# Optimization experiments

Measured on AMD Instinct MI355X. Metric: run time of the kernel, lower is better.

The kernel has to match this reference:

```python
import jax, jax.numpy as jnp
import numpy as np

N_NODE = 100000
EMB = 112
NNZ = 1000000
B = 512
L = 50
LAYERS = 2


def setup_inputs() -> dict:
    key = jax.random.key(0)
    ks = jax.random.split(key, 9)
    embedding = jax.random.normal(ks[0], (N_NODE, EMB), dtype=jnp.float32) * 0.1
    adj_vals = jax.random.uniform(ks[1], (NNZ,), dtype=jnp.float32)
    adj_rows = jax.random.randint(ks[2], (NNZ,), 0, N_NODE, dtype=jnp.int32)
    adj_cols = jax.random.randint(ks[3], (NNZ,), 0, N_NODE, dtype=jnp.int32)
    D = jax.random.normal(ks[4], (B, B), dtype=jnp.float32) * (1.0 / B)
    A = jax.random.normal(ks[5], (B, B), dtype=jnp.float32)
    session_item = jax.random.randint(ks[6], (B, L), 0, N_NODE + 1, dtype=jnp.int32)  # 0 = pad row
    session_len = jnp.floor(jax.random.uniform(ks[7], (B, 1), dtype=jnp.float32) * (L - 1)) + 1.0
    stdv = 1.0 / np.sqrt(EMB)
    w_sess = jax.random.normal(ks[8], (LAYERS, EMB, EMB), dtype=jnp.float32) * stdv
    return {"embedding": embedding, "adj_vals": adj_vals, "adj_rows": adj_rows,
            "adj_cols": adj_cols, "D": D, "A": A, "session_item": session_item,
            "session_len": session_len, "w_sess": w_sess}


def _l2_normalize(x, eps=1e-12):
    n = jnp.linalg.norm(x, axis=-1, keepdims=True)
    return x / jnp.maximum(n, eps)


def _hyperconv(embedding, adj_vals, adj_rows, adj_cols):
    # mean over layer outputs of repeated sparse.mm(adjacency, embedding)
    cur = embedding
    acc = embedding
    for _ in range(LAYERS):
        msgs = adj_vals[:, None] * cur[adj_cols]           # [nnz, E] gather
        cur = jax.ops.segment_sum(msgs, adj_rows, num_segments=N_NODE)
        acc = acc + cur
    return acc / (LAYERS + 1)


def _sessconv(item_emb, D, A, session_item, session_len, w_sess):
    pad_emb = jnp.concatenate([jnp.zeros((1, EMB), item_emb.dtype), item_emb], axis=0)
    seq_h = pad_emb[session_item]                           # [B, L, E] gather (vectorized index_select loop)
    sess = jnp.sum(seq_h, axis=1) / session_len             # [B, E] mean pool
    DA = D @ A                                              # [B, B]
    acc = sess
    for i in range(LAYERS):
        sess = sess @ w_sess[i].T                           # Linear, no bias
        sess = DA @ sess
        sess = _l2_normalize(sess)
        acc = acc + sess
    return acc / (LAYERS + 1)


def reference(embedding, adj_vals, adj_rows, adj_cols, D, A, session_item, session_len, w_sess):
    item_emb = _hyperconv(embedding, adj_vals, adj_rows, adj_cols)
    sess_emb = _sessconv(item_emb, D, A, session_item, session_len, w_sess)
    return sess_emb
```

## Files before the change

### kernel.cpp

```cpp
#include <hip/hip_runtime.h>
#include <hip/hip_bf16.h>

#define N_NODE 100000
#define EMB 112
#define EMBQ 28
#define EMBQ4 14
#define NNZ 1000000
#define BATCH 512
#define SEQL 50

typedef unsigned int uint32;

__device__ __forceinline__ unsigned short f2bf(float f) {
    uint32 u = __float_as_uint(f);
    u = (u + 0x7fffu + ((u >> 16) & 1u)) >> 16;
    return (unsigned short)u;
}
__device__ __forceinline__ uint32 pack_bf2(float x, float y) {
    return (uint32)f2bf(x) | ((uint32)f2bf(y) << 16);
}
__device__ __forceinline__ float2 unpack_bf2(uint32 p) {
    float2 r;
    r.x = __uint_as_float(p << 16);
    r.y = __uint_as_float(p & 0xffff0000u);
    return r;
}

#define NPAD 100352
#define NBUCKET 196
#define BCAP 6144
#define CHUNK 2048
#define MS_BLOCKS 489
#define MAXC 25600
#define POISON ((int)0xAAAAAAAA)

__global__ __launch_bounds__(256)
void split_prep_kernel(const int* __restrict__ rows,
                       const int* __restrict__ cols,
                       const float* __restrict__ vals,
                       int* __restrict__ cur, int2* __restrict__ tmp,
                       const float4* __restrict__ embf4,
                       uint2* __restrict__ embb2,
                       const int* __restrict__ items,
                       int* __restrict__ flags, int* __restrict__ mapv,
                       int* __restrict__ rlist, int* __restrict__ cntp) {
    __shared__ int hist[NBUCKET];
    __shared__ int lexcl[NBUCKET];
    __shared__ int gbase[NBUCKET];
    __shared__ int lcur[NBUCKET];
    __shared__ int sscan[256];
    __shared__ unsigned char sbuck[CHUNK];
    __shared__ int2 stage[CHUNK];
    int t = threadIdx.x;
    if (blockIdx.x < MS_BLOCKS) {
        int base = blockIdx.x * CHUNK;
        int m = NNZ - base; if (m > CHUNK) m = CHUNK;
        for (int j = t; j < NBUCKET; j += 256) hist[j] = 0;
        __syncthreads();
        for (int i = t; i < m; i += 256) atomicAdd(&hist[rows[base + i] >> 9], 1);
        __syncthreads();
        int v = (t < NBUCKET) ? hist[t] : 0;
        sscan[t] = v;
        __syncthreads();
#pragma unroll
        for (int d = 1; d < 256; d <<= 1) {
            int x = (t >= d) ? sscan[t - d] : 0;
            __syncthreads();
            sscan[t] += x;
            __syncthreads();
        }
        if (t < NBUCKET) {
            int e = sscan[t] - v;
            lexcl[t] = e;
            lcur[t] = e;
            gbase[t] = t * BCAP + (atomicAdd(&cur[t], v) - POISON);
        }
        __syncthreads();
        for (int i = t; i < m; i += 256) {
            int r = rows[base + i];
            int b = r >> 9;
            int p = atomicAdd(&lcur[b], 1);
            stage[p] = make_int2(cols[base + i] | ((r & 511) << 17),
                                 __float_as_int(vals[base + i]));
            sbuck[p] = (unsigned char)b;
        }
        __syncthreads();
        for (int i = t; i < m; i += 256) {
            int b = sbuck[i];
            tmp[gbase[b] + (i - lexcl[b])] = stage[i];
        }
    } else {
        int i = (blockIdx.x - MS_BLOCKS) * 256 + t;
        if (i < N_NODE * EMBQ) {
            float4 v = embf4[i];
            uint2 o;
            o.x = pack_bf2(v.x, v.y);
            o.y = pack_bf2(v.z, v.w);
            embb2[i] = o;
        }
        if (i < BATCH * SEQL) {
            int it = items[i];
            if (it > 0) {
                int old = atomicCAS(&flags[it - 1], POISON, 1);
                if (old == POISON) {
                    int rank = atomicAdd(cntp, 1) - POISON;
                    mapv[it - 1] = rank;
                    rlist[rank] = it - 1;
                }
            }
        }
    }
}

__global__ __launch_bounds__(256)
void sort_gemm_kernel(const int* __restrict__ cur, const int2* __restrict__ tmp,
                      int2* __restrict__ edges, int* __restrict__ off,
                      const float* __restrict__ D, const float* __restrict__ A,
                      float* __restrict__ DA) {
    __shared__ __align__(16) char smem[56320];
    int t = threadIdx.x;
    if (blockIdx.x < NBUCKET) {
        int* hist   = (int*)smem;
        int* scanb  = (int*)(smem + 2048);
        int* lcur   = (int*)(smem + 4096);
        int* sscan  = (int*)(smem + 6144);
        int2* stage = (int2*)(smem + 7168);
        int b = blockIdx.x;
        int base = b * BCAP;
        int cnt = cur[b] - POISON;
        for (int j = t; j < 512; j += 256) hist[j] = 0;
        __syncthreads();
        for (int i = t; i < cnt; i += 256) {
            int2 e = tmp[base + i];
            stage[i] = e;
            atomicAdd(&hist[(e.x >> 17) & 511], 1);
        }
        __syncthreads();
        int a0 = hist[2 * t], a1 = hist[2 * t + 1];
        int s = a0 + a1;
        sscan[t] = s;
        __syncthreads();
#pragma unroll
        for (int d = 1; d < 256; d <<= 1) {
            int x = (t >= d) ? sscan[t - d] : 0;
            __syncthreads();
            sscan[t] += x;
            __syncthreads();
        }
        int excl = sscan[t] - s;
        scanb[2 * t] = excl;
        scanb[2 * t + 1] = excl + a0;
        lcur[2 * t] = excl;
        lcur[2 * t + 1] = excl + a0;
        __syncthreads();
        for (int j = t; j < 512; j += 256) off[(b << 9) + j] = base + scanb[j];
        for (int i = t; i < cnt; i += 256) {
            int2 e = stage[i];
            int rl = (e.x >> 17) & 511;
            int p = atomicAdd(&lcur[rl], 1);
            edges[base + p] = make_int2(e.x & 0x1FFFF, e.y);
        }
    } else {
        float (*sDt)[36] = (float(*)[36])smem;
        float (*sA)[68] = (float(*)[68])(smem + 2304);
        int bx = blockIdx.x - NBUCKET;
        int tx = t & 15, ty = t >> 4;
        int m0 = (bx >> 3) * 32, n0 = (bx & 7) * 64;
        float acc[2][4];
#pragma unroll
        for (int i = 0; i < 2; ++i)
#pragma unroll
            for (int j = 0; j < 4; ++j) acc[i][j] = 0.0f;
        int dm = t >> 2, dk = (t & 3) * 4;
        int ak = t >> 4, an = (t & 15) * 4;
        for (int k0 = 0; k0 < BATCH; k0 += 16) {
            float4 dv;
            if (t < 128)
                dv = *(const float4*)(D + (size_t)(m0 + dm) * BATCH + k0 + dk);
            float4 av = *(const float4*)(A + (size_t)(k0 + ak) * BATCH + n0 + an);
            __syncthreads();
            if (t < 128) {
                sDt[dk + 0][dm] = dv.x;
                sDt[dk + 1][dm] = dv.y;
                sDt[dk + 2][dm] = dv.z;
                sDt[dk + 3][dm] = dv.w;
            }
            *(float4*)&sA[ak][an] = av;
            __syncthreads();
#pragma unroll
            for (int k = 0; k < 16; ++k) {
                float a0 = sDt[k][ty * 2 + 0];
                float a1 = sDt[k][ty * 2 + 1];
                float4 bv = *(const float4*)&sA[k][tx * 4];
                float br[4] = {bv.x, bv.y, bv.z, bv.w};
#pragma unroll
                for (int j = 0; j < 4; ++j) {
                    acc[0][j] += a0 * br[j];
                    acc[1][j] += a1 * br[j];
                }
            }
        }
#pragma unroll
        for (int i = 0; i < 2; ++i) {
            float4 o = make_float4(acc[i][0], acc[i][1], acc[i][2], acc[i][3]);
            *(float4*)(DA + (size_t)(m0 + ty * 2 + i) * BATCH + n0 + tx * 4) = o;
        }
    }
}

__global__ __launch_bounds__(256, 6)
void spmm_csr_kernel(const uint32* __restrict__ curb,
                     const float4* __restrict__ embf,
                     const int* __restrict__ rowptr,
                     const int* __restrict__ bcnt,
                     const int2* __restrict__ edges,
                     const int* __restrict__ rlist,
                     const int* __restrict__ cntp,
                     void* __restrict__ outm, int fuse_final) {
    int t = threadIdx.x;
    int lane16 = t & 15;
    int slot = t >> 4;
    int srcbase = t & 48;
    int idx = (blockIdx.x << 4) + slot;
    int r;
    if (rlist) {
        if (idx >= cntp[0] - POISON) return;
        r = rlist[idx];
    } else {
        r = idx;
        if (r >= N_NODE) return;
    }
    int beg = rowptr[r];
    int end = ((r & 511) == 511) ? ((r >> 9) * BCAP + (bcnt[r >> 9] - POISON))
                                 : rowptr[r + 1];
    int len = end - beg;
    int q = lane16;
    int qc = (q < EMBQ4) ? q : (EMBQ4 - 1);
    const uint4* basep = (const uint4*)curb;
    float4 accA = make_float4(0.0f, 0.0f, 0.0f, 0.0f);
    float4 accB = make_float4(0.0f, 0.0f, 0.0f, 0.0f);
    for (int b0 = 0; b0 < len; b0 += 16) {
        int m = len - b0; if (m > 16) m = 16;
        int2 e = (lane16 < m) ? edges[beg + b0 + lane16] : make_int2(0, 0);
        for (int k = 0; k < m; k += 8) {
            int   c0 = __shfl(e.x, srcbase + k + 0, 64);
            float v0 = __int_as_float(__shfl(e.y, srcbase + k + 0, 64));
            int   c1 = __shfl(e.x, srcbase + k + 1, 64);
            float v1 = __int_as_float(__shfl(e.y, srcbase + k + 1, 64));
            int   c2 = __shfl(e.x, srcbase + k + 2, 64);
            float v2 = __int_as_float(__shfl(e.y, srcbase + k + 2, 64));
            int   c3 = __shfl(e.x, srcbase + k + 3, 64);
            float v3 = __int_as_float(__shfl(e.y, srcbase + k + 3, 64));
            int   c4 = __shfl(e.x, srcbase + k + 4, 64);
            float v4 = __int_as_float(__shfl(e.y, srcbase + k + 4, 64));
            int   c5 = __shfl(e.x, srcbase + k + 5, 64);
            float v5 = __int_as_float(__shfl(e.y, srcbase + k + 5, 64));
            int   c6 = __shfl(e.x, srcbase + k + 6, 64);
            float v6 = __int_as_float(__shfl(e.y, srcbase + k + 6, 64));
            int   c7 = __shfl(e.x, srcbase + k + 7, 64);
            float v7 = __int_as_float(__shfl(e.y, srcbase + k + 7, 64));
            uint4 x0 = basep[c0 * EMBQ4 + qc];
            uint4 x1 = basep[c1 * EMBQ4 + qc];
            uint4 x2 = basep[c2 * EMBQ4 + qc];
            uint4 x3 = basep[c3 * EMBQ4 + qc];
            uint4 x4 = basep[c4 * EMBQ4 + qc];
            uint4 x5 = basep[c5 * EMBQ4 + qc];
            uint4 x6 = basep[c6 * EMBQ4 + qc];
            uint4 x7 = basep[c7 * EMBQ4 + qc];
            float2 p0a = unpack_bf2(x0.x), p0b = unpack_bf2(x0.y),
                   p0c = unpack_bf2(x0.z), p0d = unpack_bf2(x0.w);
            float2 p1a = unpack_bf2(x1.x), p1b = unpack_bf2(x1.y),
                   p1c = unpack_bf2(x1.z), p1d = unpack_bf2(x1.w);
            float2 p2a = unpack_bf2(x2.x), p2b = unpack_bf2(x2.y),
                   p2c = unpack_bf2(x2.z), p2d = unpack_bf2(x2.w);
            float2 p3a = unpack_bf2(x3.x), p3b = unpack_bf2(x3.y),
                   p3c = unpack_bf2(x3.z), p3d = unpack_bf2(x3.w);
            float2 p4a = unpack_bf2(x4.x), p4b = unpack_bf2(x4.y),
                   p4c = unpack_bf2(x4.z), p4d = unpack_bf2(x4.w);
            float2 p5a = unpack_bf2(x5.x), p5b = unpack_bf2(x5.y),
                   p5c = unpack_bf2(x5.z), p5d = unpack_bf2(x5.w);
            float2 p6a = unpack_bf2(x6.x), p6b = unpack_bf2(x6.y),
                   p6c = unpack_bf2(x6.z), p6d = unpack_bf2(x6.w);
            float2 p7a = unpack_bf2(x7.x), p7b = unpack_bf2(x7.y),
                   p7c = unpack_bf2(x7.z), p7d = unpack_bf2(x7.w);
            accA.x += v0 * p0a.x; accA.y += v0 * p0a.y;
            accA.z += v0 * p0b.x; accA.w += v0 * p0b.y;
            accB.x += v0 * p0c.x; accB.y += v0 * p0c.y;
            accB.z += v0 * p0d.x; accB.w += v0 * p0d.y;
            accA.x += v1 * p1a.x; accA.y += v1 * p1a.y;
            accA.z += v1 * p1b.x; accA.w += v1 * p1b.y;
            accB.x += v1 * p1c.x; accB.y += v1 * p1c.y;
            accB.z += v1 * p1d.x; accB.w += v1 * p1d.y;
            accA.x += v2 * p2a.x; accA.y += v2 * p2a.y;
            accA.z += v2 * p2b.x; accA.w += v2 * p2b.y;
            accB.x += v2 * p2c.x; accB.y += v2 * p2c.y;
            accB.z += v2 * p2d.x; accB.w += v2 * p2d.y;
            accA.x += v3 * p3a.x; accA.y += v3 * p3a.y;
            accA.z += v3 * p3b.x; accA.w += v3 * p3b.y;
            accB.x += v3 * p3c.x; accB.y += v3 * p3c.y;
            accB.z += v3 * p3d.x; accB.w += v3 * p3d.y;
            accA.x += v4 * p4a.x; accA.y += v4 * p4a.y;
            accA.z += v4 * p4b.x; accA.w += v4 * p4b.y;
            accB.x += v4 * p4c.x; accB.y += v4 * p4c.y;
            accB.z += v4 * p4d.x; accB.w += v4 * p4d.y;
            accA.x += v5 * p5a.x; accA.y += v5 * p5a.y;
            accA.z += v5 * p5b.x; accA.w += v5 * p5b.y;
            accB.x += v5 * p5c.x; accB.y += v5 * p5c.y;
            accB.z += v5 * p5d.x; accB.w += v5 * p5d.y;
            accA.x += v6 * p6a.x; accA.y += v6 * p6a.y;
            accA.z += v6 * p6b.x; accA.w += v6 * p6b.y;
            accB.x += v6 * p6c.x; accB.y += v6 * p6c.y;
            accB.z += v6 * p6d.x; accB.w += v6 * p6d.y;
            accA.x += v7 * p7a.x; accA.y += v7 * p7a.y;
            accA.z += v7 * p7b.x; accA.w += v7 * p7b.y;
            accB.x += v7 * p7c.x; accB.y += v7 * p7c.y;
            accB.z += v7 * p7d.x; accB.w += v7 * p7d.y;
        }
    }
    if (q < EMBQ4) {
        if (fuse_final) {
            uint4 cb = ((const uint4*)curb)[(size_t)r * EMBQ4 + q];
            float2 c0f = unpack_bf2(cb.x), c1f = unpack_bf2(cb.y),
                   c2f = unpack_bf2(cb.z), c3f = unpack_bf2(cb.w);
            float4 e0 = embf[(size_t)r * EMBQ + 2 * q];
            float4 e1 = embf[(size_t)r * EMBQ + 2 * q + 1];
            float4 r0, r1;
            r0.x = (accA.x + c0f.x + e0.x) * (1.0f / 3.0f);
            r0.y = (accA.y + c0f.y + e0.y) * (1.0f / 3.0f);
            r0.z = (accA.z + c1f.x + e0.z) * (1.0f / 3.0f);
            r0.w = (accA.w + c1f.y + e0.w) * (1.0f / 3.0f);
            r1.x = (accB.x + c2f.x + e1.x) * (1.0f / 3.0f);
            r1.y = (accB.y + c2f.y + e1.y) * (1.0f / 3.0f);
            r1.z = (accB.z + c3f.x + e1.z) * (1.0f / 3.0f);
            r1.w = (accB.w + c3f.y + e1.w) * (1.0f / 3.0f);
            ((float4*)outm)[(size_t)idx * EMBQ + 2 * q] = r0;
            ((float4*)outm)[(size_t)idx * EMBQ + 2 * q + 1] = r1;
        } else {
            uint4 o4;
            o4.x = pack_bf2(accA.x, accA.y);
            o4.y = pack_bf2(accA.z, accA.w);
            o4.z = pack_bf2(accB.x, accB.y);
            o4.w = pack_bf2(accB.z, accB.w);
            ((uint4*)outm)[(size_t)r * EMBQ4 + q] = o4;
        }
    }
}

__global__ __launch_bounds__(128)
void pool_lin_kernel(const float* __restrict__ item_c,
                     const int* __restrict__ map,
                     const int* __restrict__ items,
                     const float* __restrict__ slen,
                     const float* __restrict__ W1,
                     float* __restrict__ accb, float* __restrict__ t1) {
    __shared__ float srow[EMB];
    int b = blockIdx.x;
    int f = threadIdx.x;
    if (f < EMB) {
        float s = 0.0f;
        for (int l = 0; l < SEQL; ++l) {
            int it = items[b * SEQL + l];
            if (it > 0) s += item_c[(size_t)map[it - 1] * EMB + f];
        }
        s /= slen[b];
        srow[f] = s;
        accb[b * EMB + f] = s;
    }
    __syncthreads();
    if (f < EMB) {
        float a = 0.0f;
#pragma unroll 4
        for (int k = 0; k < EMB; ++k) a += srow[k] * W1[f * EMB + k];
        t1[b * EMB + f] = a;
    }
}

__global__ __launch_bounds__(128)
void damul_lin_kernel(const float* __restrict__ DA,
                      const float* __restrict__ t1,
                      const float* __restrict__ W2,
                      float* __restrict__ accb, float* __restrict__ t2) {
    __shared__ float srow[EMB];
    __shared__ float partial[2];
    int b = blockIdx.x;
    int j = threadIdx.x;
    float v = 0.0f;
    if (j < EMB) {
        const float* darow = DA + (size_t)b * BATCH;
        for (int k0 = 0; k0 < BATCH; k0 += 4) {
            float4 d4 = *(const float4*)(darow + k0);
            float a0 = t1[(k0 + 0) * EMB + j];
            float a1 = t1[(k0 + 1) * EMB + j];
            float a2 = t1[(k0 + 2) * EMB + j];
            float a3 = t1[(k0 + 3) * EMB + j];
            v += d4.x * a0 + d4.y * a1 + d4.z * a2 + d4.w * a3;
        }
    }
    float sq = (j < EMB) ? v * v : 0.0f;
#pragma unroll
    for (int off = 32; off > 0; off >>= 1) sq += __shfl_down(sq, off, 64);
    if ((j & 63) == 0) partial[j >> 6] = sq;
    __syncthreads();
    float inv = 1.0f / fmaxf(sqrtf(partial[0] + partial[1]), 1e-12f);
    if (j < EMB) {
        float s = v * inv;
        srow[j] = s;
        accb[b * EMB + j] += s;
    }
    __syncthreads();
    if (j < EMB) {
        float a = 0.0f;
#pragma unroll 4
        for (int k = 0; k < EMB; ++k) a += srow[k] * W2[j * EMB + k];
        t2[b * EMB + j] = a;
    }
}

__global__ __launch_bounds__(128)
void damul_out_kernel(const float* __restrict__ DA,
                      const float* __restrict__ t2,
                      const float* __restrict__ accb,
                      float* __restrict__ out) {
    __shared__ float partial[2];
    int b = blockIdx.x;
    int j = threadIdx.x;
    float v = 0.0f;
    if (j < EMB) {
        const float* darow = DA + (size_t)b * BATCH;
        for (int k0 = 0; k0 < BATCH; k0 += 4) {
            float4 d4 = *(const float4*)(darow + k0);
            float a0 = t2[(k0 + 0) * EMB + j];
            float a1 = t2[(k0 + 1) * EMB + j];
            float a2 = t2[(k0 + 2) * EMB + j];
            float a3 = t2[(k0 + 3) * EMB + j];
            v += d4.x * a0 + d4.y * a1 + d4.z * a2 + d4.w * a3;
        }
    }
    float sq = (j < EMB) ? v * v : 0.0f;
#pragma unroll
    for (int off = 32; off > 0; off >>= 1) sq += __shfl_down(sq, off, 64);
    if ((j & 63) == 0) partial[j >> 6] = sq;
    __syncthreads();
    float inv = 1.0f / fmaxf(sqrtf(partial[0] + partial[1]), 1e-12f);
    if (j < EMB) {
        float s = v * inv;
        out[b * EMB + j] = (accb[b * EMB + j] + s) * (1.0f / 3.0f);
    }
}

extern "C" void kernel_launch(void* const* d_in, const int* in_sizes, int n_in,
                              void* d_out, int out_size, void* d_ws, size_t ws_size,
                              hipStream_t stream) {
    const float* embedding = (const float*)d_in[0];
    const float* adj_vals  = (const float*)d_in[1];
    const int*   adj_rows  = (const int*)d_in[2];
    const int*   adj_cols  = (const int*)d_in[3];
    const float* D         = (const float*)d_in[4];
    const float* A         = (const float*)d_in[5];
    const int*   sess_item = (const int*)d_in[6];
    const float* sess_len  = (const float*)d_in[7];
    const float* w_sess    = (const float*)d_in[8];
    float* out = (float*)d_out;

    char* ws = (char*)d_ws;
    uint32* embb   = (uint32*)(ws);
    uint32* next1b = (uint32*)(ws + 22400000);
    int2*   edges  = (int2*)(ws + 44800000);
    int*    off    = (int*)(ws + 54433792);
    int*    mapv   = (int*)(ws + 54835200);
    int*    flags  = (int*)(ws + 55236608);
    int*    cntp   = (int*)(ws + 55638016);
    int*    curb   = (int*)(ws + 55638144);
    int*    rlist  = (int*)(ws + 55639168);
    float*  item_c = (float*)(ws + 55741568);
    int2*   etmp   = (int2*)(ws + 55741568);
    float*  DA     = (float*)(ws + 67210368);
    float*  t1     = (float*)(ws + 68258944);
    float*  t2     = (float*)(ws + 68488320);
    float*  accb   = (float*)(ws + 68717696);


    {
        int conv_blocks = (N_NODE * EMBQ + 255) / 256;
        split_prep_kernel<<<MS_BLOCKS + conv_blocks, 256, 0, stream>>>(
            adj_rows, adj_cols, adj_vals, curb, etmp,
            (const float4*)embedding, (uint2*)embb,
            sess_item, flags, mapv, rlist, cntp);
    }

    sort_gemm_kernel<<<NBUCKET + 128, 256, 0, stream>>>(curb, etmp, edges, off,
                                                        D, A, DA);

    {
        int grid1 = (N_NODE + 15) / 16;
        spmm_csr_kernel<<<grid1, 256, 0, stream>>>(embb, nullptr, off, curb,
                                                   edges, nullptr, nullptr,
                                                   next1b, 0);
        int grid2 = (MAXC + 15) / 16;
        spmm_csr_kernel<<<grid2, 256, 0, stream>>>(next1b, (const float4*)embedding,
                                                   off, curb, edges, rlist, cntp,
                                                   item_c, 1);
    }

    pool_lin_kernel<<<BATCH, 128, 0, stream>>>(item_c, mapv, sess_item, sess_len,
                                               w_sess, accb, t1);
    damul_lin_kernel<<<BATCH, 128, 0, stream>>>(DA, t1, w_sess + EMB * EMB,
                                                accb, t2);
    damul_out_kernel<<<BATCH, 128, 0, stream>>>(DA, t2, accb, out);
}
```

Before: 268.8 us.

## Pad bf16 embedding rows to 128 elements for aligned SpMM gathers

Stores the bf16 embedding and intermediate layer rows padded from 112 to 128 elements (256 bytes) with zeroed tail, so each 16-lane group gathers a full aligned row without clamping the lane index. The gather address becomes a shift, and loads are 256-byte aligned. The workspace is reshuffled to fit the larger buffers, and item_c now aliases the embedding buffer, which is dead by then. Launch bounds raise the occupancy target from 6 to 8 blocks. The trade-off is about 14% more bytes per gathered row.

```diff
diff --git a/kernel.cpp b/kernel.cpp
--- a/kernel.cpp
+++ b/kernel.cpp
@@ -5,6 +5,8 @@
 #define EMB 112
 #define EMBQ 28
 #define EMBQ4 14
+#define EMBP4 16
+#define EMBP2 32
 #define NNZ 1000000
 #define BATCH 512
 #define SEQL 50
@@ -91,11 +93,17 @@
         }
     } else {
         int i = (blockIdx.x - MS_BLOCKS) * 256 + t;
-        if (i < N_NODE * EMBQ) {
-            float4 v = embf4[i];
+        if (i < N_NODE * EMBP2) {
+            int row = i >> 5, u = i & 31;
             uint2 o;
-            o.x = pack_bf2(v.x, v.y);
-            o.y = pack_bf2(v.z, v.w);
+            if (u < EMBQ) {
+                float4 v = embf4[row * EMBQ + u];
+                o.x = pack_bf2(v.x, v.y);
+                o.y = pack_bf2(v.z, v.w);
+            } else {
+                o.x = 0u;
+                o.y = 0u;
+            }
             embb2[i] = o;
         }
         if (i < BATCH * SEQL) {
@@ -208,7 +216,7 @@
     }
 }
 
-__global__ __launch_bounds__(256, 6)
+__global__ __launch_bounds__(256, 8)
 void spmm_csr_kernel(const uint32* __restrict__ curb,
                      const float4* __restrict__ embf,
                      const int* __restrict__ rowptr,
@@ -235,7 +243,6 @@
                                  : rowptr[r + 1];
     int len = end - beg;
     int q = lane16;
-    int qc = (q < EMBQ4) ? q : (EMBQ4 - 1);
     const uint4* basep = (const uint4*)curb;
     float4 accA = make_float4(0.0f, 0.0f, 0.0f, 0.0f);
     float4 accB = make_float4(0.0f, 0.0f, 0.0f, 0.0f);
@@ -259,14 +266,14 @@
             float v6 = __int_as_float(__shfl(e.y, srcbase + k + 6, 64));
             int   c7 = __shfl(e.x, srcbase + k + 7, 64);
             float v7 = __int_as_float(__shfl(e.y, srcbase + k + 7, 64));
-            uint4 x0 = basep[c0 * EMBQ4 + qc];
-            uint4 x1 = basep[c1 * EMBQ4 + qc];
-            uint4 x2 = basep[c2 * EMBQ4 + qc];
-            uint4 x3 = basep[c3 * EMBQ4 + qc];
-            uint4 x4 = basep[c4 * EMBQ4 + qc];
-            uint4 x5 = basep[c5 * EMBQ4 + qc];
-            uint4 x6 = basep[c6 * EMBQ4 + qc];
-            uint4 x7 = basep[c7 * EMBQ4 + qc];
+            uint4 x0 = basep[(c0 << 4) + q];
+            uint4 x1 = basep[(c1 << 4) + q];
+            uint4 x2 = basep[(c2 << 4) + q];
+            uint4 x3 = basep[(c3 << 4) + q];
+            uint4 x4 = basep[(c4 << 4) + q];
+            uint4 x5 = basep[(c5 << 4) + q];
+            uint4 x6 = basep[(c6 << 4) + q];
+            uint4 x7 = basep[(c7 << 4) + q];
             float2 p0a = unpack_bf2(x0.x), p0b = unpack_bf2(x0.y),
                    p0c = unpack_bf2(x0.z), p0d = unpack_bf2(x0.w);
             float2 p1a = unpack_bf2(x1.x), p1b = unpack_bf2(x1.y),
@@ -317,9 +324,9 @@
             accB.z += v7 * p7d.x; accB.w += v7 * p7d.y;
         }
     }
-    if (q < EMBQ4) {
-        if (fuse_final) {
-            uint4 cb = ((const uint4*)curb)[(size_t)r * EMBQ4 + q];
+    if (fuse_final) {
+        if (q < EMBQ4) {
+            uint4 cb = ((const uint4*)curb)[((size_t)r << 4) + q];
             float2 c0f = unpack_bf2(cb.x), c1f = unpack_bf2(cb.y),
                    c2f = unpack_bf2(cb.z), c3f = unpack_bf2(cb.w);
             float4 e0 = embf[(size_t)r * EMBQ + 2 * q];
@@ -335,14 +342,14 @@
             r1.w = (accB.w + c3f.y + e1.w) * (1.0f / 3.0f);
             ((float4*)outm)[(size_t)idx * EMBQ + 2 * q] = r0;
             ((float4*)outm)[(size_t)idx * EMBQ + 2 * q + 1] = r1;
-        } else {
-            uint4 o4;
-            o4.x = pack_bf2(accA.x, accA.y);
-            o4.y = pack_bf2(accA.z, accA.w);
-            o4.z = pack_bf2(accB.x, accB.y);
-            o4.w = pack_bf2(accB.z, accB.w);
-            ((uint4*)outm)[(size_t)r * EMBQ4 + q] = o4;
-        }
+        }
+    } else {
+        uint4 o4;
+        o4.x = pack_bf2(accA.x, accA.y);
+        o4.y = pack_bf2(accA.z, accA.w);
+        o4.z = pack_bf2(accB.x, accB.y);
+        o4.w = pack_bf2(accB.z, accB.w);
+        ((uint4*)outm)[((size_t)r << 4) + q] = o4;
     }
 }
 
@@ -464,24 +471,24 @@
 
     char* ws = (char*)d_ws;
     uint32* embb   = (uint32*)(ws);
-    uint32* next1b = (uint32*)(ws + 22400000);
-    int2*   edges  = (int2*)(ws + 44800000);
-    int*    off    = (int*)(ws + 54433792);
-    int*    mapv   = (int*)(ws + 54835200);
-    int*    flags  = (int*)(ws + 55236608);
-    int*    cntp   = (int*)(ws + 55638016);
-    int*    curb   = (int*)(ws + 55638144);
-    int*    rlist  = (int*)(ws + 55639168);
-    float*  item_c = (float*)(ws + 55741568);
-    int2*   etmp   = (int2*)(ws + 55741568);
-    float*  DA     = (float*)(ws + 67210368);
-    float*  t1     = (float*)(ws + 68258944);
-    float*  t2     = (float*)(ws + 68488320);
-    float*  accb   = (float*)(ws + 68717696);
+    float*  item_c = (float*)(ws);
+    uint32* next1b = (uint32*)(ws + 25600000);
+    int2*   etmp   = (int2*)(ws + 25600000);
+    int2*   edges  = (int2*)(ws + 51200000);
+    int*    off    = (int*)(ws + 60833792);
+    int*    mapv   = (int*)(ws + 61235200);
+    int*    flags  = (int*)(ws + 61636608);
+    int*    cntp   = (int*)(ws + 62038016);
+    int*    curb   = (int*)(ws + 62038144);
+    int*    rlist  = (int*)(ws + 62039168);
+    float*  DA     = (float*)(ws + 62141568);
+    float*  t1     = (float*)(ws + 63190144);
+    float*  t2     = (float*)(ws + 63419520);
+    float*  accb   = (float*)(ws + 63648896);
 
 
     {
-        int conv_blocks = (N_NODE * EMBQ + 255) / 256;
+        int conv_blocks = (N_NODE * EMBP2 + 255) / 256;
         split_prep_kernel<<<MS_BLOCKS + conv_blocks, 256, 0, stream>>>(
             adj_rows, adj_cols, adj_vals, curb, etmp,
             (const float4*)embedding, (uint2*)embb,
```

New measurement: 310.7 us. 1.16x slower.
